# Kernel optimization log

Measured on AMD Instinct MI355X. Metric: run time of the kernel, lower is better.

The kernel has to match this reference:

```python
import jax, jax.numpy as jnp
import numpy as np

NUM_Q_HEADS = 64
NUM_KV_HEADS = 8
HEAD_DIM = 64
HIDDEN = 2880
SLIDING_WINDOW = 128
ROPE_WAVELENGTH = 10000.0
NEG_INF = jnp.float32(-1e9)


def _rope(x, start_index=0):
    # x: (b, s, n, h). yarn with scaling_factor=1.0 == standard RoPE (split-half rotate).
    s, h = x.shape[1], x.shape[-1]
    inv_freq = 1.0 / (ROPE_WAVELENGTH ** (jnp.arange(0, h, 2, dtype=jnp.float32) / h))
    pos = jnp.arange(s, dtype=jnp.float32) + start_index
    freqs = pos[:, None] * inv_freq[None, :]  # (s, h/2)
    cos = jnp.concatenate([jnp.cos(freqs), jnp.cos(freqs)], axis=-1)[None, :, None, :]
    sin = jnp.concatenate([jnp.sin(freqs), jnp.sin(freqs)], axis=-1)[None, :, None, :]
    x1, x2 = jnp.split(x, 2, axis=-1)
    rot = jnp.concatenate([-x2, x1], axis=-1)
    return x * cos + rot * sin


def setup_inputs() -> dict:
    key = jax.random.key(0)
    ks = jax.random.split(key, 9)
    b, s = 1, 2048
    scale = 0.02
    hidden_states = jax.random.normal(ks[0], (b, s, HIDDEN), jnp.float32)
    Wq = jax.random.normal(ks[1], (HIDDEN, NUM_Q_HEADS, HEAD_DIM), jnp.float32) * scale
    Wk = jax.random.normal(ks[2], (HIDDEN, NUM_KV_HEADS, HEAD_DIM), jnp.float32) * scale
    Wv = jax.random.normal(ks[3], (HIDDEN, NUM_KV_HEADS, HEAD_DIM), jnp.float32) * scale
    Wo = jax.random.normal(ks[4], (NUM_Q_HEADS, HEAD_DIM, HIDDEN), jnp.float32) * scale
    bq = jnp.zeros((NUM_Q_HEADS, HEAD_DIM), jnp.float32)
    bk = jnp.zeros((NUM_KV_HEADS, HEAD_DIM), jnp.float32)
    bv = jnp.zeros((NUM_KV_HEADS, HEAD_DIM), jnp.float32)
    bo = jnp.zeros((HIDDEN,), jnp.float32)
    sinks = jax.random.normal(ks[5], (NUM_Q_HEADS,), jnp.float32) * 0.05
    attention_mask = jnp.tril(jnp.ones((s, s), bool))[None]  # causal, (b, q, k)
    return dict(hidden_states=hidden_states, Wq=Wq, bq=bq, Wk=Wk, bk=bk, Wv=Wv,
                bv=bv, Wo=Wo, bo=bo, sinks=sinks, attention_mask=attention_mask)


def reference(hidden_states, Wq, bq, Wk, bk, Wv, bv, Wo, bo, sinks, attention_mask):
    b, s, _ = hidden_states.shape
    inv_norm = 1.0 / np.sqrt(HEAD_DIM).astype(np.float32)
    # QKV projections (EinsumDense with bias)
    q = jnp.einsum('bqm,muh->bquh', hidden_states, Wq) + bq
    k = jnp.einsum('bkm,mvh->bkvh', hidden_states, Wk) + bk
    v = jnp.einsum('bkm,mvh->bkvh', hidden_states, Wv) + bv
    # rotary_dim == head_dim (even), so RoPE applies to the full head dim
    q = _rope(q)
    k = _rope(k)
    # GQA: repeat kv heads
    groups = NUM_Q_HEADS // NUM_KV_HEADS
    k = jnp.repeat(k, groups, axis=2)
    v = jnp.repeat(v, groups, axis=2)
    scores = jnp.einsum('bquh,bkuh->buqk', q, k) * inv_norm
    # sliding-window mask: keep kv_pos >= q_pos - window
    qpos = jnp.arange(s)
    swin = qpos[None, :] >= qpos[:, None] - SLIDING_WINDOW  # (q, k)
    scores = jnp.where(swin[None, None], scores, NEG_INF)
    scores = jnp.where(attention_mask[:, None], scores, NEG_INF)
    # sink-token logit per head appended as extra kv column
    sink = jnp.broadcast_to(sinks.reshape(1, NUM_Q_HEADS, 1, 1), (b, NUM_Q_HEADS, s, 1))
    logits = jnp.concatenate([scores, sink], axis=-1)
    m = jax.lax.stop_gradient(jnp.max(logits, axis=-1, keepdims=True))
    probs = jax.nn.softmax(logits - m, axis=-1)[..., :-1]  # drop sink column
    attn = jnp.einsum('buqk,bkuh->bquh', probs, v)
    return jnp.einsum('bquh,uhm->bqm', attn, Wo) + bo
```

## Files before the change

### kernel.cpp

```cpp
#include <hip/hip_runtime.h>
#include <cstdint>

typedef __attribute__((ext_vector_type(4))) float f32x4;
typedef __attribute__((ext_vector_type(8))) short bf16x8;

#define HIDDEN 2880
#define SEQ 2048
#define QKV_N 5120
#define WIN 128

__device__ __forceinline__ ushort f2bf(float f) {
  uint32_t u = __builtin_bit_cast(uint32_t, f);
  u += 0x7fff + ((u >> 16) & 1);
  return (ushort)(u >> 16);
}
__device__ __forceinline__ float bf2f(ushort h) {
  uint32_t u = ((uint32_t)h) << 16;
  return __builtin_bit_cast(float, u);
}

__device__ __forceinline__ void tconv_tile(const float* __restrict__ in, ushort* __restrict__ out,
                                           int C, int out_ld, int out_row_off,
                                           int bx, int by, int t, ushort (*tile)[68]) {
  int c0 = bx * 64, r0 = by * 64;
  int lr = t >> 4;
  int lc = (t & 15) * 4;
#pragma unroll
  for (int i = 0; i < 4; ++i) {
    float4 v = *(const float4*)&in[(size_t)(r0 + i * 16 + lr) * C + c0 + lc];
    ushort4 o;
    o.x = f2bf(v.x); o.y = f2bf(v.y); o.z = f2bf(v.z); o.w = f2bf(v.w);
    *(ushort4*)&tile[i * 16 + lr][lc] = o;
  }
  __syncthreads();
  int rr0 = (t & 7) * 8;
#pragma unroll
  for (int i2 = 0; i2 < 2; ++i2) {
    int cc = i2 * 32 + (t >> 3);
    bf16x8 o;
#pragma unroll
    for (int j = 0; j < 8; ++j) o[j] = (short)tile[rr0 + j][cc];
    *(bf16x8*)&out[(size_t)(out_row_off + c0 + cc) * out_ld + r0 + rr0] = o;
  }
}

__global__ __launch_bounds__(256) void prep_kernel(
    const float* __restrict__ hs, const float* __restrict__ Wq, const float* __restrict__ Wk,
    const float* __restrict__ Wv, const float* __restrict__ Wo,
    const float* __restrict__ bq, const float* __restrict__ bk, const float* __restrict__ bv,
    ushort* __restrict__ hs_bf, ushort* __restrict__ wqkv_t, ushort* __restrict__ wo_t,
    float* __restrict__ bias_all, float2* __restrict__ tab) {
  __shared__ ushort tile[64][68];
  const int b = blockIdx.x, t = threadIdx.x;
  if (b < 2880) {
    int i = (b * 256 + t) * 8;
    float4 a = *(const float4*)(hs + i);
    float4 c = *(const float4*)(hs + i + 4);
    bf16x8 o;
    o[0] = (short)f2bf(a.x); o[1] = (short)f2bf(a.y); o[2] = (short)f2bf(a.z); o[3] = (short)f2bf(a.w);
    o[4] = (short)f2bf(c.x); o[5] = (short)f2bf(c.y); o[6] = (short)f2bf(c.z); o[7] = (short)f2bf(c.w);
    *(bf16x8*)(hs_bf + i) = o;
  } else if (b < 5760) {
    int idx = b - 2880;
    tconv_tile(Wq, wqkv_t, 4096, 2880, 0, idx & 63, idx >> 6, t, tile);
  } else if (b < 6120) {
    int idx = b - 5760;
    tconv_tile(Wk, wqkv_t, 512, 2880, 4096, idx & 7, idx >> 3, t, tile);
  } else if (b < 6480) {
    int idx = b - 6120;
    tconv_tile(Wv, wqkv_t, 512, 2880, 4608, idx & 7, idx >> 3, t, tile);
  } else if (b < 9360) {
    int idx = b - 6480;
    tconv_tile(Wo, wo_t, 2880, 4096, 0, idx % 45, idx / 45, t, tile);
  } else if (b < 9380) {
    int i = (b - 9360) * 256 + t;
    if (i < QKV_N) {
      float v = (i < 4096) ? bq[i] : (i < 4608) ? bk[i - 4096] : bv[i - 4608];
      bias_all[i] = v;
    }
  } else {
    int i = (b - 9380) * 256 + t;
    int s = i >> 5, d = i & 31;
    float inv = powf(10000.0f, -(float)d / 32.0f);
    float f = (float)s * inv;
    tab[i] = make_float2(cosf(f), sinf(f));
  }
}

__global__ __launch_bounds__(256) void vt_kernel(const ushort* __restrict__ qkv, ushort* __restrict__ vt) {
  __shared__ ushort tile[64][80];
  int kv0 = blockIdx.x * 64, d0 = blockIdx.y * 64;
  int t = threadIdx.x;
#pragma unroll
  for (int p = 0; p < 2; ++p) {
    int lr = p * 32 + (t >> 3);
    *(bf16x8*)&tile[lr][(t & 7) * 8] =
        *(const bf16x8*)&qkv[(size_t)(kv0 + lr) * QKV_N + 4608 + d0 + (t & 7) * 8];
  }
  __syncthreads();
#pragma unroll
  for (int p = 0; p < 2; ++p) {
    int dl = p * 32 + (t >> 3);
    bf16x8 o;
#pragma unroll
    for (int jj = 0; jj < 8; ++jj) o[jj] = (short)tile[(t & 7) * 8 + jj][dl];
    *(bf16x8*)&vt[(size_t)(d0 + dl) * 2048 + kv0 + (t & 7) * 8] = o;
  }
}

#define LGKM0()                                              \
  do {                                                       \
    asm volatile("s_waitcnt lgkmcnt(0)" ::: "memory");       \
    __builtin_amdgcn_sched_barrier(0);                       \
  } while (0)
#define WAITV0() asm volatile("s_waitcnt vmcnt(0)" ::: "memory")
#define BAR() __builtin_amdgcn_s_barrier()

template <int BN, bool OUT_BF16>
__global__ __launch_bounds__(256, 2) void gemm4w_kernel(
    const ushort* __restrict__ A, const ushort* __restrict__ Bt,
    const float* __restrict__ bias, void* __restrict__ Cv,
    int K, int lda, int ldb, int ldc) {
  constexpr int NFRAG = BN / 32;
  constexpr int BHALF = BN * 64;
  constexpr int BCHUNKS = BHALF / 1024;
  constexpr int BUFBYTES = 16384 + 2 * BHALF;
  __shared__ __align__(16) char ldsbuf[2 * BUFBYTES];

  const int cpx = gridDim.x >> 3;
  const int wg = ((int)blockIdx.x & 7) * cpx + ((int)blockIdx.x >> 3);
  const int mtile = wg & 15, ntile = wg >> 4;
  const int m0 = mtile * 128, n0 = ntile * BN;

  const int tid = threadIdx.x, wv = tid >> 6, l = tid & 63;
  const int wm = wv >> 1, wn = wv & 1;
  const int r = l & 15, g = l >> 4;

  const int c = l ^ ((l >> 3) & 3);
  const ushort* gA0 = A + (size_t)(m0 + (c >> 2)) * lda + (c & 3) * 8;
  const ushort* gB0 = Bt + (size_t)(n0 + (c >> 2)) * ldb + (c & 3) * 8;

  const int gsw = (g * 16) ^ (((r >> 1) & 3) << 4);
  const int aOff = (wm * 64 + r) * 64 + gsw;
  const int bOff = (wn * (NFRAG * 16) + r) * 64 + gsw;

  auto sA = [&](int nb, int kg, int kh) {
#pragma unroll
    for (int j = 0; j < 2; ++j) {
      int cid = j * 4 + wv;
      __builtin_amdgcn_global_load_lds(
          (const __attribute__((address_space(1))) void*)(const void*)(gA0 + (size_t)cid * 16 * lda + kg),
          (__attribute__((address_space(3))) void*)&ldsbuf[nb * BUFBYTES + kh * 8192 + cid * 1024], 16, 0, 0);
    }
  };
  auto sB = [&](int nb, int kg, int kh) {
#pragma unroll
    for (int j = 0; j < (BCHUNKS + 3) / 4; ++j) {
      int cid = j * 4 + wv;
      if (cid < BCHUNKS)
        __builtin_amdgcn_global_load_lds(
            (const __attribute__((address_space(1))) void*)(const void*)(gB0 + (size_t)cid * 16 * ldb + kg),
            (__attribute__((address_space(3))) void*)&ldsbuf[nb * BUFBYTES + 16384 + kh * BHALF + cid * 1024],
            16, 0, 0);
    }
  };

  f32x4 acc[4][NFRAG] = {};
  const int nt = K >> 6;

  sA(0, 0, 0); sA(0, 32, 1); sB(0, 0, 0); sB(0, 32, 1);
  WAITV0();
  BAR();

  for (int t = 0; t < nt; ++t) {
    const int bufOff = (t & 1) * BUFBYTES;
    const int nb = (t & 1) ^ 1;
    if (t + 1 < nt) {
      const int kn = (t + 1) * 64;
      sA(nb, kn, 0); sA(nb, kn + 32, 1);
      sB(nb, kn, 0); sB(nb, kn + 32, 1);
    }
#pragma unroll
    for (int kh = 0; kh < 2; ++kh) {
      bf16x8 aq[4], bq[NFRAG];
#pragma unroll
      for (int nf = 0; nf < NFRAG; ++nf)
        bq[nf] = *(const bf16x8*)&ldsbuf[bufOff + 16384 + kh * BHALF + bOff + nf * 1024];
#pragma unroll
      for (int mi = 0; mi < 4; ++mi)
        aq[mi] = *(const bf16x8*)&ldsbuf[bufOff + kh * 8192 + aOff + mi * 1024];
      LGKM0();
      __builtin_amdgcn_s_setprio(1);
#pragma unroll
      for (int mi = 0; mi < 4; ++mi)
#pragma unroll
        for (int nf = 0; nf < NFRAG; ++nf)
          acc[mi][nf] = __builtin_amdgcn_mfma_f32_16x16x32_bf16(aq[mi], bq[nf], acc[mi][nf], 0, 0, 0);
      __builtin_amdgcn_s_setprio(0);
    }
    WAITV0();
    BAR();
  }

#pragma unroll
  for (int mf2 = 0; mf2 < 4; ++mf2) {
#pragma unroll
    for (int nf = 0; nf < NFRAG; ++nf) {
      int cc = n0 + wn * (NFRAG * 16) + nf * 16 + r;
      float b = bias[cc];
#pragma unroll
      for (int j = 0; j < 4; ++j) {
        int rrow = m0 + wm * 64 + mf2 * 16 + g * 4 + j;
        float v = acc[mf2][nf][j] + b;
        if (OUT_BF16) ((ushort*)Cv)[(size_t)rrow * ldc + cc] = f2bf(v);
        else ((float*)Cv)[(size_t)rrow * ldc + cc] = v;
      }
    }
  }
}

__global__ __launch_bounds__(512, 4) void attn_kernel(
    const ushort* __restrict__ qkv, const ushort* __restrict__ vt,
    const float* __restrict__ sinks, const float2* __restrict__ tab,
    ushort* __restrict__ out) {
  __shared__ __align__(16) char lds[54272];
  const int kh = blockIdx.y;
  const int q0 = blockIdx.x * 32;
  const int kvw0 = q0 - 128;
  const int tid = threadIdx.x, w = tid >> 6, l = tid & 63;
  const int r = l & 15, g = l >> 4;
  const int h = kh * 8 + w;

  if (tid < 256) ((uint32_t*)(lds + 40960))[tid] = 0;

#pragma unroll
  for (int it = 0; it < 4; ++it) {
    int c = it * 512 + tid;
    if (c < 640) {
      int row = c >> 2, ch = c & 3;
      int kv = kvw0 + row;
      bf16x8 v1 = {}, v2 = {};
      if (kv >= 0) {
        const ushort* kb = &qkv[(size_t)kv * QKV_N + 4096 + kh * 64 + ch * 8];
        bf16x8 x1 = *(const bf16x8*)kb;
        bf16x8 x2 = *(const bf16x8*)(kb + 32);
#pragma unroll
        for (int i = 0; i < 8; ++i) {
          float2 cs = tab[(kv << 5) + ch * 8 + i];
          float a = bf2f((ushort)x1[i]), b = bf2f((ushort)x2[i]);
          v1[i] = (short)f2bf(a * cs.x - b * cs.y);
          v2[i] = (short)f2bf(b * cs.x + a * cs.y);
        }
      }
      int b1 = (row * 128 + ch * 16) ^ ((row & 7) << 4);
      int b2 = (row * 128 + (ch + 4) * 16) ^ ((row & 7) << 4);
      *(bf16x8*)(lds + b1) = v1;
      *(bf16x8*)(lds + b2) = v2;
    } else if (c < 1920) {
      int cv = c - 640;
      int row = cv / 20, ch = cv - (cv / 20) * 20;
      int kv = kvw0 + ch * 8;
      bf16x8 vv = {};
      if (kv >= 0) vv = *(const bf16x8*)&vt[(size_t)(kh * 64 + row) * 2048 + kv];
      int byte = (row * 320 + ch * 16) ^ ((row & 7) << 4);
      *(bf16x8*)(lds + 20480 + byte) = vv;
    }
  }
  __syncthreads();

  char* Pw = lds + 41984 + w * 1536;
  const float snk = sinks[h];

#pragma unroll
  for (int si = 0; si < 2; ++si) {
    const ushort* qb = &qkv[(size_t)(q0 + si * 16 + r) * QKV_N + h * 64 + g * 8];
    bf16x8 qf0 = *(const bf16x8*)qb;
    bf16x8 qf1 = *(const bf16x8*)(qb + 32);
    {
      int s = q0 + si * 16 + r;
      bf16x8 t0, t1;
#pragma unroll
      for (int i = 0; i < 8; ++i) {
        float2 cs = tab[(s << 5) + g * 8 + i];
        float a = bf2f((ushort)qf0[i]), b = bf2f((ushort)qf1[i]);
        t0[i] = (short)f2bf(a * cs.x - b * cs.y);
        t1[i] = (short)f2bf(b * cs.x + a * cs.y);
      }
      qf0 = t0; qf1 = t1;
    }

    f32x4 S[9];
    float mx[4] = {-3e30f, -3e30f, -3e30f, -3e30f};
#pragma unroll
    for (int tt = 0; tt < 9; ++tt) {
      int kvloc = (si + tt) * 16 + r;
      int b0 = (kvloc * 128 + g * 16) ^ ((kvloc & 7) << 4);
      int b1 = (kvloc * 128 + 64 + g * 16) ^ ((kvloc & 7) << 4);
      bf16x8 kf0 = *(const bf16x8*)(lds + b0);
      bf16x8 kf1 = *(const bf16x8*)(lds + b1);
      f32x4 s = {};
      s = __builtin_amdgcn_mfma_f32_16x16x32_bf16(qf0, kf0, s, 0, 0, 0);
      s = __builtin_amdgcn_mfma_f32_16x16x32_bf16(qf1, kf1, s, 0, 0, 0);
      int kvc = kvw0 + kvloc;
#pragma unroll
      for (int j = 0; j < 4; ++j) {
        int qr = q0 + si * 16 + g * 4 + j;
        bool valid = (kvc >= 0) && (kvc <= qr) && (kvc >= qr - WIN);
        float v = valid ? s[j] * 0.125f : -1e30f;
        s[j] = v;
        mx[j] = fmaxf(mx[j], v);
      }
      S[tt] = s;
    }
#pragma unroll
    for (int off = 1; off < 16; off <<= 1)
#pragma unroll
      for (int j = 0; j < 4; ++j) mx[j] = fmaxf(mx[j], __shfl_xor(mx[j], off, 64));
    float m[4], sum[4] = {0, 0, 0, 0};
#pragma unroll
    for (int j = 0; j < 4; ++j) m[j] = fmaxf(mx[j], snk);
#pragma unroll
    for (int tt = 0; tt < 9; ++tt)
#pragma unroll
      for (int j = 0; j < 4; ++j) {
        float p = (S[tt][j] > -1e29f) ? __expf(S[tt][j] - m[j]) : 0.0f;
        S[tt][j] = p;
        sum[j] += p;
      }
#pragma unroll
    for (int off = 1; off < 16; off <<= 1)
#pragma unroll
      for (int j = 0; j < 4; ++j) sum[j] += __shfl_xor(sum[j], off, 64);
    float rinv[4];
#pragma unroll
    for (int j = 0; j < 4; ++j) rinv[j] = 1.0f / (sum[j] + __expf(snk - m[j]));

    f32x4 acc[4] = {};
#pragma unroll
    for (int ks = 0; ks < 5; ++ks) {
#pragma unroll
      for (int c2 = 0; c2 < 2; ++c2) {
        int tt = 2 * ks + c2;
#pragma unroll
        for (int j = 0; j < 4; ++j) {
          float pv = (tt <= 8) ? S[tt][j] * rinv[j] : 0.0f;
          *(ushort*)(Pw + ((g * 4 + j) * 48 + c2 * 16 + r) * 2) = f2bf(pv);
        }
      }
      bf16x8 pa = *(const bf16x8*)(Pw + (r * 48 + g * 8) * 2);
#pragma unroll
      for (int ni = 0; ni < 4; ++ni) {
        int row = ni * 16 + r;
        int byte = (row * 320 + (si * 16 + ks * 32 + g * 8) * 2) ^ ((row & 7) << 4);
        bf16x8 vb = *(const bf16x8*)(lds + 20480 + byte);
        acc[ni] = __builtin_amdgcn_mfma_f32_16x16x32_bf16(pa, vb, acc[ni], 0, 0, 0);
      }
    }
#pragma unroll
    for (int ni = 0; ni < 4; ++ni)
#pragma unroll
      for (int j = 0; j < 4; ++j)
        out[(size_t)(q0 + si * 16 + g * 4 + j) * 4096 + h * 64 + ni * 16 + r] = f2bf(acc[ni][j]);
  }
}

extern "C" void kernel_launch(void* const* d_in, const int* in_sizes, int n_in,
                              void* d_out, int out_size, void* d_ws, size_t ws_size,
                              hipStream_t stream) {
  const float* hs = (const float*)d_in[0];
  const float* Wq = (const float*)d_in[1];
  const float* bq = (const float*)d_in[2];
  const float* Wk = (const float*)d_in[3];
  const float* bk = (const float*)d_in[4];
  const float* Wv = (const float*)d_in[5];
  const float* bv = (const float*)d_in[6];
  const float* Wo = (const float*)d_in[7];
  const float* bo = (const float*)d_in[8];
  const float* sinks = (const float*)d_in[9];
  float* out = (float*)d_out;

  char* ws = (char*)d_ws;
  ushort* hs_bf   = (ushort*)(ws + 0);
  ushort* vt_g    = (ushort*)(ws + 0);
  ushort* wqkv_t  = (ushort*)(ws + 11796480);
  ushort* attn    = (ushort*)(ws + 11796480);
  ushort* wo_t    = (ushort*)(ws + 41287680);
  ushort* qkv     = (ushort*)(ws + 66453504);
  float*  bias_all= (float*)(ws + 87425024);
  float2* tab     = (float2*)(ws + 87445504);

  prep_kernel<<<9636, 256, 0, stream>>>(hs, Wq, Wk, Wv, Wo, bq, bk, bv,
                                        hs_bf, wqkv_t, wo_t, bias_all, tab);

  gemm4w_kernel<160, true><<<512, 256, 0, stream>>>(hs_bf, wqkv_t, bias_all, qkv,
                                                    2880, 2880, 2880, 5120);
  vt_kernel<<<dim3(32, 8), 256, 0, stream>>>(qkv, vt_g);
  attn_kernel<<<dim3(64, 8), 512, 0, stream>>>(qkv, vt_g, sinks, tab, attn);
  gemm4w_kernel<160, false><<<288, 256, 0, stream>>>(attn, wo_t, bo, out,
                                                     4096, 4096, 4096, 2880);
}
```

Measured before the change: 192.1 us.

## Use 256x256-tile 8-wave GEMM kernel for QKV projection

Adds a dedicated GEMM kernel with 256x256 output tiles, 512 threads and double-buffered 64KB LDS stages fed by direct global-to-LDS loads, and uses it for the QKV projection. Larger tiles raise arithmetic intensity and cut redundant global/LDS traffic per MFMA. In exchange the grid shrinks to 160 blocks, leaving many CUs idle, and the large LDS footprint limits occupancy.

```diff
diff --git a/kernel.cpp b/kernel.cpp
--- a/kernel.cpp
+++ b/kernel.cpp
@@ -114,7 +114,122 @@
     __builtin_amdgcn_sched_barrier(0);                       \
   } while (0)
 #define WAITV0() asm volatile("s_waitcnt vmcnt(0)" ::: "memory")
+#define WAITV4() asm volatile("s_waitcnt vmcnt(4)" ::: "memory")
 #define BAR() __builtin_amdgcn_s_barrier()
+
+__global__ __launch_bounds__(512, 2) void gemm256_kernel(
+    const ushort* __restrict__ A, const ushort* __restrict__ Bt,
+    const float* __restrict__ bias, ushort* __restrict__ Cv,
+    int K, int lda, int ldb, int ldc) {
+  constexpr int BUFBYTES = 65536;
+  __shared__ __align__(16) char ldsbuf[2 * BUFBYTES];
+
+  const int cpx = gridDim.x >> 3;
+  const int wg = ((int)blockIdx.x & 7) * cpx + ((int)blockIdx.x >> 3);
+  const int mtile = wg / 20, ntile = wg - mtile * 20;
+  const int m0 = mtile * 256, n0 = ntile * 256;
+
+  const int tid = threadIdx.x, wv = tid >> 6, l = tid & 63;
+  const int wm = wv >> 2, wn = wv & 3;
+  const int r = l & 15, g = l >> 4;
+
+  const int c = l ^ ((l >> 3) & 3);
+  const ushort* gA0 = A + (size_t)(m0 + (c >> 2)) * lda + (c & 3) * 8;
+  const ushort* gB0 = Bt + (size_t)(n0 + (c >> 2)) * ldb + (c & 3) * 8;
+
+  const int gsw = (g * 16) ^ (((r >> 1) & 3) << 4);
+  const int aOff = (wm * 128 + r) * 64 + gsw;
+  const int bOff = (wn * 64 + r) * 64 + gsw;
+
+  auto sA = [&](int nb, int kg, int kh) {
+#pragma unroll
+    for (int j = 0; j < 2; ++j) {
+      int cid = j * 8 + wv;
+      __builtin_amdgcn_global_load_lds(
+          (const __attribute__((address_space(1))) void*)(const void*)(gA0 + (size_t)cid * 16 * lda + kg),
+          (__attribute__((address_space(3))) void*)&ldsbuf[nb * BUFBYTES + kh * 16384 + cid * 1024], 16, 0, 0);
+    }
+  };
+  auto sB = [&](int nb, int kg, int kh) {
+#pragma unroll
+    for (int j = 0; j < 2; ++j) {
+      int cid = j * 8 + wv;
+      __builtin_amdgcn_global_load_lds(
+          (const __attribute__((address_space(1))) void*)(const void*)(gB0 + (size_t)cid * 16 * ldb + kg),
+          (__attribute__((address_space(3))) void*)&ldsbuf[nb * BUFBYTES + 32768 + kh * 16384 + cid * 1024],
+          16, 0, 0);
+    }
+  };
+
+#define READ_B256(KH)                                                             \
+  _Pragma("unroll") for (int nf = 0; nf < 4; ++nf)                                \
+      bq[nf] = *(const bf16x8*)&ldsbuf[bufOff + 32768 + (KH)*16384 + bOff + nf * 1024];
+#define READ_A256(KH, MF0)                                                        \
+  _Pragma("unroll") for (int i2 = 0; i2 < 4; ++i2)                                \
+      aq[i2] = *(const bf16x8*)&ldsbuf[bufOff + (KH)*16384 + aOff + ((MF0) + i2) * 1024];
+#define MFMA16(MB)                                                                \
+  __builtin_amdgcn_s_setprio(1);                                                  \
+  _Pragma("unroll") for (int i2 = 0; i2 < 4; ++i2) {                              \
+    _Pragma("unroll") for (int nf = 0; nf < 4; ++nf)                              \
+        acc[(MB) + i2][nf] = __builtin_amdgcn_mfma_f32_16x16x32_bf16(             \
+            aq[i2], bq[nf], acc[(MB) + i2][nf], 0, 0, 0);                         \
+  }                                                                               \
+  __builtin_amdgcn_s_setprio(0)
+
+  f32x4 acc[8][4] = {};
+  const int nt = K >> 6;
+
+  sA(0, 0, 0); sB(0, 0, 0);
+  sA(0, 32, 1); sB(0, 32, 1);
+  WAITV4();
+  BAR();
+
+  for (int t = 0; t < nt; ++t) {
+    const int bufOff = (t & 1) * BUFBYTES;
+    const int nb = (t & 1) ^ 1;
+    const int kn = (t + 1) << 6;
+    const bool more = (t + 1 < nt);
+    bf16x8 aq[4], bq[4];
+
+    READ_B256(0); READ_A256(0, 0);
+    if (more) sA(nb, kn, 0);
+    BAR(); LGKM0();
+    MFMA16(0);
+    BAR();
+    READ_A256(0, 4);
+    if (more) { sB(nb, kn, 0); WAITV4(); } else { WAITV0(); }
+    BAR(); LGKM0();
+    MFMA16(4);
+    BAR();
+    READ_B256(1); READ_A256(1, 0);
+    if (more) sA(nb, kn + 32, 1);
+    BAR(); LGKM0();
+    MFMA16(0);
+    BAR();
+    READ_A256(1, 4);
+    if (more) { sB(nb, kn + 32, 1); WAITV4(); } else { WAITV0(); }
+    BAR(); LGKM0();
+    MFMA16(4);
+    BAR();
+  }
+
+#pragma unroll
+  for (int mf2 = 0; mf2 < 8; ++mf2) {
+#pragma unroll
+    for (int nf = 0; nf < 4; ++nf) {
+      int cc = n0 + wn * 64 + nf * 16 + r;
+      float b = bias[cc];
+#pragma unroll
+      for (int j = 0; j < 4; ++j) {
+        int rrow = m0 + wm * 128 + mf2 * 16 + g * 4 + j;
+        Cv[(size_t)rrow * ldc + cc] = f2bf(acc[mf2][nf][j] + b);
+      }
+    }
+  }
+#undef READ_B256
+#undef READ_A256
+#undef MFMA16
+}
 
 template <int BN, bool OUT_BF16>
 __global__ __launch_bounds__(256, 2) void gemm4w_kernel(
@@ -392,8 +507,8 @@
   prep_kernel<<<9636, 256, 0, stream>>>(hs, Wq, Wk, Wv, Wo, bq, bk, bv,
                                         hs_bf, wqkv_t, wo_t, bias_all, tab);
 
-  gemm4w_kernel<160, true><<<512, 256, 0, stream>>>(hs_bf, wqkv_t, bias_all, qkv,
-                                                    2880, 2880, 2880, 5120);
+  gemm256_kernel<<<160, 512, 0, stream>>>(hs_bf, wqkv_t, bias_all, qkv,
+                                          2880, 2880, 2880, 5120);
   vt_kernel<<<dim3(32, 8), 256, 0, stream>>>(qkv, vt_g);
   attn_kernel<<<dim3(64, 8), 512, 0, stream>>>(qkv, vt_g, sinks, tab, attn);
   gemm4w_kernel<160, false><<<288, 256, 0, stream>>>(attn, wo_t, bo, out,
```

Measured after the change: 208.6 us. +8.6%, slower.
